# Optimization experiments

Measured on AMD Instinct MI355X. Metric: run time of the kernel, lower is better.

Reference implementation:

```python
import jax, jax.numpy as jnp
import numpy as np

# Segmented tensor-product configuration (matches init_kwargs)
NUM_SEG = 32   # segments per operand
MUL = 128      # multiplicity ('u' axis) of operand0 / output segments
D = 3          # irrep dimension (2l+1 with l=1) for i, j, k axes
NUM_PATHS = 64
BATCH = 2048


def setup_inputs() -> dict:
    key = jax.random.key(0)
    k0, k1, k2, k3, k4, k5 = jax.random.split(key, 6)
    x0 = jax.random.normal(k0, (BATCH, NUM_SEG * MUL * D), dtype=jnp.float32)
    x1 = jax.random.normal(k1, (BATCH, NUM_SEG * D), dtype=jnp.float32)
    coeff = jax.random.normal(k2, (NUM_PATHS, D, D, D), dtype=jnp.float32)
    idx0 = jax.random.randint(k3, (NUM_PATHS,), 0, NUM_SEG, dtype=jnp.int32)
    idx1 = jax.random.randint(k4, (NUM_PATHS,), 0, NUM_SEG, dtype=jnp.int32)
    idx2 = jax.random.randint(k5, (NUM_PATHS,), 0, NUM_SEG, dtype=jnp.int32)
    return {"x0": x0, "x1": x1, "coeff": coeff,
            "idx0": idx0, "idx1": idx1, "idx2": idx2}


def reference(x0, x1, coeff, idx0, idx1, idx2):
    # Segmented CG tensor product:
    #   out[seg2][u,k] += sum_{paths p with idx2[p]==seg2}
    #       sum_ij x0[idx0[p]][u,i] * x1[idx1[p]][j] * coeff[p][i,j,k]
    B = x0.shape[0]
    x0s = x0.reshape(B, NUM_SEG, MUL, D)   # 'ui' segments
    x1s = x1.reshape(B, NUM_SEG, D)        # 'j' segments
    # gather input segments per path
    x0p = x0s[:, idx0]                     # (B, P, MUL, D)
    x1p = x1s[:, idx1]                     # (B, P, D)
    # per-path contraction with path coefficients, path axis first for scatter
    contrib = jnp.einsum('bpui,bpj,pijk->pbuk', x0p, x1p, coeff)
    # scatter-add contributions into output segments
    out_seg = jax.ops.segment_sum(contrib, idx2, num_segments=NUM_SEG)  # (S, B, MUL, D)
    out = jnp.transpose(out_seg, (1, 0, 2, 3)).reshape(B, NUM_SEG * MUL * D)
    return out
```

## Files before the change

### kernel.cpp

```cpp
#include <hip/hip_runtime.h>

#define NUM_SEG 32
#define MUL 128
#define D 3
#define NUM_PATHS 64
#define ROW (NUM_SEG * MUL * D)
#define SEGF (MUL * D)
#define SEG_HF 192

typedef float v2f __attribute__((ext_vector_type(2)));
typedef float v4f __attribute__((ext_vector_type(4)));

__global__ __launch_bounds__(64) void ftp_setup(
    const float* __restrict__ x1, const float* __restrict__ coeff,
    const int* __restrict__ idx0, const int* __restrict__ idx1,
    const int* __restrict__ idx2,
    unsigned int* __restrict__ sched, float* __restrict__ m)
{
    const int tid = threadIdx.x;
    if (blockIdx.x == 0) {
        __shared__ int lcnt[NUM_SEG];
        __shared__ int loff[NUM_SEG];
        __shared__ int lperm[NUM_SEG];
        __shared__ unsigned short lent[NUM_PATHS];
        if (tid < NUM_SEG) lcnt[tid] = 0;
        __syncthreads();
        const int p   = tid;
        const int s2  = idx2[p];
        const int pos = atomicAdd(&lcnt[s2], 1);
        __syncthreads();
        if (tid == 0) {
            int off = 0;
            for (int s = 0; s < NUM_SEG; ++s) { loff[s] = off; off += lcnt[s]; }
            int perm[NUM_SEG];
            for (int s = 0; s < NUM_SEG; ++s) perm[s] = s;
            for (int i = 1; i < NUM_SEG; ++i) {
                int v = perm[i], cv = lcnt[v], j = i - 1;
                while (j >= 0 && lcnt[perm[j]] < cv) { perm[j + 1] = perm[j]; --j; }
                perm[j + 1] = v;
            }
            for (int s = 0; s < NUM_SEG; ++s) lperm[s] = perm[s];
        }
        __syncthreads();
        lent[loff[s2] + pos] = (unsigned short)(idx0[p] | (p << 8));
        __syncthreads();
        if (tid < NUM_SEG) {
            const int sg = lperm[tid];
            sched[tid] = (unsigned)lcnt[sg] | ((unsigned)loff[sg] << 8)
                       | ((unsigned)sg << 16);
        }
        if (tid < NUM_PATHS / 2) {
            sched[NUM_SEG + tid] = (unsigned)lent[2 * tid]
                                 | ((unsigned)lent[2 * tid + 1] << 16);
        }
    } else {
        const int b = blockIdx.x - 1;
        const int p = tid;
        const float* xr = x1 + (size_t)b * (NUM_SEG * D) + idx1[p] * D;
        const float j0 = xr[0], j1 = xr[1], j2 = xr[2];
        const float* cf = coeff + p * 27;
        float* mp = m + (size_t)b * (NUM_PATHS * 9) + p * 9;
        #pragma unroll
        for (int i = 0; i < D; ++i)
            #pragma unroll
            for (int k = 0; k < D; ++k)
                mp[i * 3 + k] = j0 * cf[i * 9 + k]
                              + j1 * cf[i * 9 + 3 + k]
                              + j2 * cf[i * 9 + 6 + k];
    }
}

__global__ __launch_bounds__(256, 6) void ftp_main(
    const float* __restrict__ x0, const unsigned int* __restrict__ sched,
    const float* __restrict__ m, float* __restrict__ out)
{
    const int bid = blockIdx.x;
    const int b   = bid >> 1;
    const int h   = bid & 1;
    const int tid = threadIdx.x;

    __shared__ float s_x0[NUM_SEG * SEG_HF];
    __shared__ float s_m[NUM_PATHS][9];
    __shared__ unsigned int s_sched[NUM_SEG];
    __shared__ unsigned int s_entw[NUM_PATHS / 2];

    const v4f* __restrict__ srcb = (const v4f*)(x0 + (size_t)b * ROW);
    #pragma unroll
    for (int j = 0; j < 6; ++j) {
        const int F   = j * 256 + tid;
        const int seg = F / 48;
        const int in4 = F - seg * 48;
        const v4f* gp = srcb + seg * 96 + h * 48 + in4;
        __builtin_amdgcn_global_load_lds(
            (const __attribute__((address_space(1))) void*)gp,
            (__attribute__((address_space(3))) void*)((v4f*)s_x0 + F),
            16, 0, 0);
    }

    if (tid < 144) {
        const v4f* mg = (const v4f*)(m + (size_t)b * (NUM_PATHS * 9));
        ((v4f*)s_m)[tid] = mg[tid];
    } else if (tid < 176) {
        s_sched[tid - 144] = sched[tid - 144];
    } else if (tid < 208) {
        s_entw[tid - 176] = sched[NUM_SEG + (tid - 176)];
    }
    __syncthreads();

    const int q  = tid & 31;
    const int ss = tid >> 5;
    const unsigned short* s_ent = (const unsigned short*)s_entw;
    float* __restrict__ ob = out + (size_t)b * ROW + h * SEG_HF + q * 6;

    #pragma unroll
    for (int si = 0; si < 4; ++si) {
        const unsigned sc = s_sched[ss + si * 8];
        const int n   = sc & 255;
        const int off = (sc >> 8) & 255;
        const int s   = sc >> 16;
        float a00 = 0, a01 = 0, a02 = 0, a10 = 0, a11 = 0, a12 = 0;
        for (int t = 0; t < n; ++t) {
            const int e = s_ent[off + t];
            const float* xs = s_x0 + (e & 255) * SEG_HF + q * 6;
            const float u00 = xs[0], u01 = xs[1], u02 = xs[2];
            const float u10 = xs[3], u11 = xs[4], u12 = xs[5];
            const float* mm = s_m[e >> 8];
            a00 += u00 * mm[0] + u01 * mm[3] + u02 * mm[6];
            a01 += u00 * mm[1] + u01 * mm[4] + u02 * mm[7];
            a02 += u00 * mm[2] + u01 * mm[5] + u02 * mm[8];
            a10 += u10 * mm[0] + u11 * mm[3] + u12 * mm[6];
            a11 += u10 * mm[1] + u11 * mm[4] + u12 * mm[7];
            a12 += u10 * mm[2] + u11 * mm[5] + u12 * mm[8];
        }
        float* o = ob + s * SEGF;
        v2f O0 = {a00, a01}, O1 = {a02, a10}, O2 = {a11, a12};
        *(v2f*)(o + 0) = O0;
        *(v2f*)(o + 2) = O1;
        *(v2f*)(o + 4) = O2;
    }
}

#define HALF_F4 1536

__global__ __launch_bounds__(256) void ftp_kernel(
    const float* __restrict__ x0, const float* __restrict__ x1,
    const float* __restrict__ coeff, const int* __restrict__ idx0,
    const int* __restrict__ idx1, const int* __restrict__ idx2,
    float* __restrict__ out)
{
    const int bid = blockIdx.x;
    const int b   = bid >> 1;
    const int h   = bid & 1;
    const int tid = threadIdx.x;

    __shared__ v4f   s_x0[HALF_F4];
    __shared__ float s_m[NUM_PATHS][9];
    __shared__ unsigned short s_pe[NUM_SEG][NUM_PATHS];
    __shared__ int   s_cnt[NUM_SEG];

    if (tid < NUM_SEG) s_cnt[tid] = 0;
    __syncthreads();

    const v4f* __restrict__ src = (const v4f*)(x0 + (size_t)b * ROW);
    #pragma unroll
    for (int j = 0; j < 6; ++j) {
        const int f     = j * 256 + tid;
        const int seg   = f / 48;
        const int inner = f - seg * 48;
        s_x0[f] = src[seg * 96 + h * 48 + inner];
    }

    if (tid < NUM_PATHS) {
        const int p  = tid;
        const int s0 = idx0[p];
        const int i1 = idx1[p];
        const int s2 = idx2[p];
        const int pos = atomicAdd(&s_cnt[s2], 1);
        s_pe[s2][pos] = (unsigned short)(s0 | (p << 8));

        const float* xr = x1 + (size_t)b * (NUM_SEG * D) + i1 * D;
        const float j0 = xr[0], j1 = xr[1], j2 = xr[2];
        const float* cf = coeff + p * 27;
        #pragma unroll
        for (int i = 0; i < D; ++i)
            #pragma unroll
            for (int k = 0; k < D; ++k)
                s_m[p][i * 3 + k] = j0 * cf[i * 9 + k]
                                  + j1 * cf[i * 9 + 3 + k]
                                  + j2 * cf[i * 9 + 6 + k];
    }
    __syncthreads();

    const int q  = tid & 31;
    const int ss = tid >> 5;
    float* __restrict__ ob = out + (size_t)b * ROW + h * SEG_HF + q * 6;
    const float* __restrict__ sx = (const float*)s_x0;

    #pragma unroll
    for (int si = 0; si < 4; ++si) {
        const int s = ss + si * 8;
        float a00 = 0, a01 = 0, a02 = 0, a10 = 0, a11 = 0, a12 = 0;
        const int n = s_cnt[s];
        for (int t = 0; t < n; ++t) {
            const int e = s_pe[s][t];
            const float* xs = sx + (e & 255) * SEG_HF + q * 6;
            const float u00 = xs[0], u01 = xs[1], u02 = xs[2];
            const float u10 = xs[3], u11 = xs[4], u12 = xs[5];
            const float* mm = s_m[e >> 8];
            a00 += u00 * mm[0] + u01 * mm[3] + u02 * mm[6];
            a01 += u00 * mm[1] + u01 * mm[4] + u02 * mm[7];
            a02 += u00 * mm[2] + u01 * mm[5] + u02 * mm[8];
            a10 += u10 * mm[0] + u11 * mm[3] + u12 * mm[6];
            a11 += u10 * mm[1] + u11 * mm[4] + u12 * mm[7];
            a12 += u10 * mm[2] + u11 * mm[5] + u12 * mm[8];
        }
        float* o = ob + s * SEGF;
        v2f O0 = {a00, a01}, O1 = {a02, a10}, O2 = {a11, a12};
        *(v2f*)(o + 0) = O0;
        *(v2f*)(o + 2) = O1;
        *(v2f*)(o + 4) = O2;
    }
}

extern "C" void kernel_launch(void* const* d_in, const int* in_sizes, int n_in,
                              void* d_out, int out_size, void* d_ws, size_t ws_size,
                              hipStream_t stream) {
    const float* x0    = (const float*)d_in[0];
    const float* x1    = (const float*)d_in[1];
    const float* coeff = (const float*)d_in[2];
    const int*   idx0  = (const int*)d_in[3];
    const int*   idx1  = (const int*)d_in[4];
    const int*   idx2  = (const int*)d_in[5];
    float* out = (float*)d_out;

    const int B = in_sizes[0] / ROW;

    const size_t schedBytes = (size_t)(NUM_SEG + NUM_PATHS / 2) * sizeof(unsigned int);
    const size_t schedPad   = (schedBytes + 255) & ~(size_t)255;
    const size_t mBytes     = (size_t)B * NUM_PATHS * 9 * sizeof(float);

    if (ws_size >= schedPad + mBytes) {
        unsigned int* sched = (unsigned int*)d_ws;
        float*        m     = (float*)((char*)d_ws + schedPad);
        ftp_setup<<<B + 1, 64, 0, stream>>>(x1, coeff, idx0, idx1, idx2, sched, m);
        ftp_main<<<B * 2, 256, 0, stream>>>(x0, sched, m, out);
    } else {
        ftp_kernel<<<B * 2, 256, 0, stream>>>(x0, x1, coeff, idx0, idx1, idx2, out);
    }
}
```

Before: 216.0 us.

## Make main kernel persistent with double-buffered async LDS staging of tiles

The main kernel becomes persistent, with the grid capped at 512 blocks that loop over batch-half tiles. While computing the current tile, each block prefetches the next tile's x0 slice and path matrices into a second LDS buffer using global_load_lds, synchronised with vmcnt waits and barriers. The per-path matrix buffer is padded to a stride of 16 floats so it can be staged with direct-to-LDS loads, and segment ranks are interleaved so per-warp work is more even. The aim is to hide global load latency behind compute. In exchange, LDS per block doubles, far fewer blocks are resident, and the padded matrix buffer adds global traffic.

```diff
diff --git a/kernel.cpp b/kernel.cpp
--- a/kernel.cpp
+++ b/kernel.cpp
@@ -7,6 +7,8 @@
 #define ROW (NUM_SEG * MUL * D)
 #define SEGF (MUL * D)
 #define SEG_HF 192
+#define NBLK 512
+#define M_STRIDE 16
 
 typedef float v2f __attribute__((ext_vector_type(2)));
 typedef float v4f __attribute__((ext_vector_type(4)));
@@ -59,7 +61,7 @@
         const float* xr = x1 + (size_t)b * (NUM_SEG * D) + idx1[p] * D;
         const float j0 = xr[0], j1 = xr[1], j2 = xr[2];
         const float* cf = coeff + p * 27;
-        float* mp = m + (size_t)b * (NUM_PATHS * 9) + p * 9;
+        float* mp = m + (size_t)b * (NUM_PATHS * M_STRIDE) + p * M_STRIDE;
         #pragma unroll
         for (int i = 0; i < D; ++i)
             #pragma unroll
@@ -70,73 +72,103 @@
     }
 }
 
-__global__ __launch_bounds__(256, 6) void ftp_main(
-    const float* __restrict__ x0, const unsigned int* __restrict__ sched,
-    const float* __restrict__ m, float* __restrict__ out)
-{
-    const int bid = blockIdx.x;
-    const int b   = bid >> 1;
-    const int h   = bid & 1;
-    const int tid = threadIdx.x;
-
-    __shared__ float s_x0[NUM_SEG * SEG_HF];
-    __shared__ float s_m[NUM_PATHS][9];
-    __shared__ unsigned int s_sched[NUM_SEG];
-    __shared__ unsigned int s_entw[NUM_PATHS / 2];
-
-    const v4f* __restrict__ srcb = (const v4f*)(x0 + (size_t)b * ROW);
+__device__ __forceinline__ void stage_tile(
+    const float* __restrict__ x0, const float* __restrict__ m,
+    int t, float* s_x0buf, float* s_mbuf, int tid)
+{
+    const int b = t >> 1, h = t & 1;
+    const v4f* src = (const v4f*)(x0 + (size_t)b * ROW);
     #pragma unroll
     for (int j = 0; j < 6; ++j) {
         const int F   = j * 256 + tid;
         const int seg = F / 48;
         const int in4 = F - seg * 48;
-        const v4f* gp = srcb + seg * 96 + h * 48 + in4;
         __builtin_amdgcn_global_load_lds(
-            (const __attribute__((address_space(1))) void*)gp,
-            (__attribute__((address_space(3))) void*)((v4f*)s_x0 + F),
+            (const __attribute__((address_space(1))) void*)(src + seg * 96 + h * 48 + in4),
+            (__attribute__((address_space(3))) void*)((v4f*)s_x0buf + F),
             16, 0, 0);
     }
-
-    if (tid < 144) {
-        const v4f* mg = (const v4f*)(m + (size_t)b * (NUM_PATHS * 9));
-        ((v4f*)s_m)[tid] = mg[tid];
-    } else if (tid < 176) {
-        s_sched[tid - 144] = sched[tid - 144];
-    } else if (tid < 208) {
-        s_entw[tid - 176] = sched[NUM_SEG + (tid - 176)];
-    }
-    __syncthreads();
-
-    const int q  = tid & 31;
-    const int ss = tid >> 5;
+    const float* msrc = m + (size_t)b * (NUM_PATHS * M_STRIDE);
+    #pragma unroll
+    for (int j = 0; j < 4; ++j) {
+        const int F = j * 256 + tid;
+        __builtin_amdgcn_global_load_lds(
+            (const __attribute__((address_space(1))) void*)(msrc + F),
+            (__attribute__((address_space(3))) void*)(s_mbuf + F),
+            4, 0, 0);
+    }
+}
+
+__global__ __launch_bounds__(256) void ftp_main(
+    const float* __restrict__ x0, const unsigned int* __restrict__ sched,
+    const float* __restrict__ m, float* __restrict__ out, int B)
+{
+    __shared__ __align__(16) float s_x0[2][NUM_SEG * SEG_HF];
+    __shared__ __align__(16) float s_m[2][NUM_PATHS * M_STRIDE];
+    __shared__ unsigned int s_sched[NUM_SEG];
+    __shared__ unsigned int s_entw[NUM_PATHS / 2];
+
+    const int tid = threadIdx.x;
+    if (tid < 32)      s_sched[tid]      = sched[tid];
+    else if (tid < 64) s_entw[tid - 32]  = sched[tid];
+
+    const int nt = B * 2;
+    int t = blockIdx.x;
+    if (t >= nt) return;
+
+    stage_tile(x0, m, t, s_x0[0], s_m[0], tid);
+    asm volatile("s_waitcnt lgkmcnt(0)" ::: "memory");
+
+    const int g = tid >> 5;
+    const int q = tid & 31;
     const unsigned short* s_ent = (const unsigned short*)s_entw;
-    float* __restrict__ ob = out + (size_t)b * ROW + h * SEG_HF + q * 6;
-
-    #pragma unroll
-    for (int si = 0; si < 4; ++si) {
-        const unsigned sc = s_sched[ss + si * 8];
-        const int n   = sc & 255;
-        const int off = (sc >> 8) & 255;
-        const int s   = sc >> 16;
-        float a00 = 0, a01 = 0, a02 = 0, a10 = 0, a11 = 0, a12 = 0;
-        for (int t = 0; t < n; ++t) {
-            const int e = s_ent[off + t];
-            const float* xs = s_x0 + (e & 255) * SEG_HF + q * 6;
-            const float u00 = xs[0], u01 = xs[1], u02 = xs[2];
-            const float u10 = xs[3], u11 = xs[4], u12 = xs[5];
-            const float* mm = s_m[e >> 8];
-            a00 += u00 * mm[0] + u01 * mm[3] + u02 * mm[6];
-            a01 += u00 * mm[1] + u01 * mm[4] + u02 * mm[7];
-            a02 += u00 * mm[2] + u01 * mm[5] + u02 * mm[8];
-            a10 += u10 * mm[0] + u11 * mm[3] + u12 * mm[6];
-            a11 += u10 * mm[1] + u11 * mm[4] + u12 * mm[7];
-            a12 += u10 * mm[2] + u11 * mm[5] + u12 * mm[8];
-        }
-        float* o = ob + s * SEGF;
-        v2f O0 = {a00, a01}, O1 = {a02, a10}, O2 = {a11, a12};
-        *(v2f*)(o + 0) = O0;
-        *(v2f*)(o + 2) = O1;
-        *(v2f*)(o + 4) = O2;
+    int cur = 0;
+
+    while (t < nt) {
+        const int tn = t + NBLK;
+        if (tn < nt) {
+            stage_tile(x0, m, tn, s_x0[cur ^ 1], s_m[cur ^ 1], tid);
+            asm volatile("s_waitcnt vmcnt(10)" ::: "memory");
+        } else {
+            asm volatile("s_waitcnt vmcnt(0)" ::: "memory");
+        }
+        __builtin_amdgcn_s_barrier();
+
+        const float* sx = s_x0[cur];
+        const float* sm = s_m[cur];
+        const int b = t >> 1, h = t & 1;
+        float* __restrict__ ob = out + (size_t)b * ROW + h * SEG_HF + q * 6;
+
+        #pragma unroll
+        for (int r = 0; r < 4; ++r) {
+            const int rank = (r == 0) ? g : (r == 1) ? (15 - g)
+                           : (r == 2) ? (16 + g) : (31 - g);
+            const unsigned sc = s_sched[rank];
+            const int n   = sc & 255;
+            const int off = (sc >> 8) & 255;
+            const int s   = sc >> 16;
+            float a00 = 0, a01 = 0, a02 = 0, a10 = 0, a11 = 0, a12 = 0;
+            for (int ei = 0; ei < n; ++ei) {
+                const int e = s_ent[off + ei];
+                const float* xs = sx + (e & 255) * SEG_HF + q * 6;
+                const float u00 = xs[0], u01 = xs[1], u02 = xs[2];
+                const float u10 = xs[3], u11 = xs[4], u12 = xs[5];
+                const float* mm = sm + (e >> 8) * M_STRIDE;
+                a00 += u00 * mm[0] + u01 * mm[3] + u02 * mm[6];
+                a01 += u00 * mm[1] + u01 * mm[4] + u02 * mm[7];
+                a02 += u00 * mm[2] + u01 * mm[5] + u02 * mm[8];
+                a10 += u10 * mm[0] + u11 * mm[3] + u12 * mm[6];
+                a11 += u10 * mm[1] + u11 * mm[4] + u12 * mm[7];
+                a12 += u10 * mm[2] + u11 * mm[5] + u12 * mm[8];
+            }
+            float* o = ob + s * SEGF;
+            v2f O0 = {a00, a01}, O1 = {a02, a10}, O2 = {a11, a12};
+            *(v2f*)(o + 0) = O0;
+            *(v2f*)(o + 2) = O1;
+            *(v2f*)(o + 4) = O2;
+        }
+        __builtin_amdgcn_s_barrier();
+        t = tn; cur ^= 1;
     }
 }
 
@@ -237,13 +269,14 @@
 
     const size_t schedBytes = (size_t)(NUM_SEG + NUM_PATHS / 2) * sizeof(unsigned int);
     const size_t schedPad   = (schedBytes + 255) & ~(size_t)255;
-    const size_t mBytes     = (size_t)B * NUM_PATHS * 9 * sizeof(float);
+    const size_t mBytes     = (size_t)B * NUM_PATHS * M_STRIDE * sizeof(float);
 
     if (ws_size >= schedPad + mBytes) {
         unsigned int* sched = (unsigned int*)d_ws;
         float*        m     = (float*)((char*)d_ws + schedPad);
         ftp_setup<<<B + 1, 64, 0, stream>>>(x1, coeff, idx0, idx1, idx2, sched, m);
-        ftp_main<<<B * 2, 256, 0, stream>>>(x0, sched, m, out);
+        const int grid = (B * 2 < NBLK) ? B * 2 : NBLK;
+        ftp_main<<<grid, 256, 0, stream>>>(x0, sched, m, out, B);
     } else {
         ftp_kernel<<<B * 2, 256, 0, stream>>>(x0, x1, coeff, idx0, idx1, idx2, out);
     }
```

New measurement: 209.8 us. 2.9% less time.
